# Optimization experiments

Measured on AMD Instinct MI355X. Metric: run time of the kernel, lower is better.

## Reference

```python
import jax, jax.numpy as jnp
import numpy as np

HIDDEN = 1000
IN_DIM = 1024


def setup_inputs() -> dict:
    key = jax.random.key(0)
    ks = jax.random.split(key, 9)
    s = 0.05
    return {
        "x": jax.random.normal(ks[0], (64, 128, IN_DIM), dtype=jnp.float32),
        "W1": jax.random.normal(ks[1], (IN_DIM, 4 * HIDDEN), dtype=jnp.float32) * s,
        "U1": jax.random.normal(ks[2], (HIDDEN, 4 * HIDDEN), dtype=jnp.float32) * s,
        "b1": jnp.zeros((4 * HIDDEN,), dtype=jnp.float32),
        "W2": jax.random.normal(ks[3], (HIDDEN, 4 * HIDDEN), dtype=jnp.float32) * s,
        "U2": jax.random.normal(ks[4], (HIDDEN, 4 * HIDDEN), dtype=jnp.float32) * s,
        "b2": jnp.zeros((4 * HIDDEN,), dtype=jnp.float32),
        "Wo": jax.random.normal(ks[5], (HIDDEN, 6), dtype=jnp.float32) * s,
        "bo": jnp.zeros((6,), dtype=jnp.float32),
    }


def _lstm_step(h, c, z):
    # Keras LSTMCell gate order: i, f, g(cell), o
    i, f, g, o = jnp.split(z, 4, axis=-1)
    i = jax.nn.sigmoid(i)
    f = jax.nn.sigmoid(f)
    o = jax.nn.sigmoid(o)
    c_new = f * c + i * jnp.tanh(g)
    h_new = o * jnp.tanh(c_new)
    return h_new, c_new


def reference(x, W1, U1, b1, W2, U2, b2, Wo, bo):
    B = x.shape[0]
    xs = jnp.swapaxes(x, 0, 1)  # [T, B, D]

    def step(carry, xt):
        h1, c1, h2, c2 = carry
        z1 = xt @ W1 + h1 @ U1 + b1
        h1, c1 = _lstm_step(h1, c1, z1)
        z2 = h1 @ W2 + h2 @ U2 + b2
        h2, c2 = _lstm_step(h2, c2, z2)
        return (h1, c1, h2, c2), None

    zeros = jnp.zeros((B, HIDDEN), dtype=x.dtype)
    (h1, c1, h2, c2), _ = jax.lax.scan(step, (zeros, zeros, zeros, zeros), xs)
    # RNN(return_sequences=False) returns last top-cell hidden state
    return h2 @ Wo + bo
```

## Files before the change

kernel.cpp:

```cpp
#include <hip/hip_runtime.h>
#include <hip/hip_bf16.h>

#define TT 128
#define DD 1024
#define HH 1000
#define NBLK 252
#define RING 16

typedef float f32x4 __attribute__((ext_vector_type(4)));
typedef __bf16 bf16x8 __attribute__((ext_vector_type(8)));

__device__ __forceinline__ bf16x8 asbf(f32x4 v) { return __builtin_bit_cast(bf16x8, v); }

__device__ __forceinline__ void ld_a(bf16x8* d, const char* p) {
    asm volatile("global_load_dwordx4 %0, %1, off sc0" : "=v"(*d) : "v"(p));
}
__device__ __forceinline__ void st_byp(char* p, bf16x8 v) {
    asm volatile("global_store_dwordx4 %0, %1, off sc0 sc1" :: "v"(p), "v"(v) : "memory");
}
__device__ __forceinline__ void st_ctl(unsigned* p, unsigned v) {
    asm volatile("global_store_dword %0, %1, off sc0 sc1" :: "v"(p), "v"(v) : "memory");
}

#define AT_RLX __ATOMIC_RELAXED
#define SC_AGT __HIP_MEMORY_SCOPE_AGENT

__global__ void zero_ws(unsigned int* __restrict__ p, int nwords) {
    int i = blockIdx.x * blockDim.x + threadIdx.x;
    if (i < nwords) p[i] = 0u;
}

__global__ void cast_x(const float* __restrict__ x, __bf16* __restrict__ xfh) {
    int gid = blockIdx.x * 256 + threadIdx.x;
    int lane = gid & 63;
    int mt = (gid >> 6) & 3;
    int ks = (gid >> 8) & 31;
    int t  = gid >> 13;
    int row = mt * 16 + (lane & 15);
    int k0  = ks * 32 + (lane >> 4) * 8;
    const float* sp = x + ((size_t)row * TT + t) * 1024 + k0;
    float4 v0 = *(const float4*)sp;
    float4 v1 = *(const float4*)(sp + 4);
    float f[8] = {v0.x, v0.y, v0.z, v0.w, v1.x, v1.y, v1.z, v1.w};
    bf16x8 hv;
#pragma unroll
    for (int j = 0; j < 8; ++j) hv[j] = (__bf16)f[j];
    ((bf16x8*)xfh)[gid] = hv;
}

__global__ __launch_bounds__(256) void pack_w2(
    const float* __restrict__ W1, const float* __restrict__ U1,
    const float* __restrict__ W2, const float* __restrict__ U2,
    __bf16* __restrict__ w1h, __bf16* __restrict__ w2h)
{
    int nt = blockIdx.x;
    int layer = blockIdx.y;
    const float* R1 = layer ? W2 : W1;
    const float* R2 = layer ? U2 : U1;
    int k1v = layer ? HH : 1024;
    __bf16* dh = layer ? w2h : w1h;
    int tid = threadIdx.x;

    __shared__ float lt[64][21];

    int kk = tid >> 2, g = tid & 3;
    for (int c = 0; c < 32; ++c) {
        int k = c * 64 + kk;
        float4 v = {0.f, 0.f, 0.f, 0.f};
        if (k < 1024) {
            if (k < k1v) v = *(const float4*)(R1 + (size_t)k * 4000 + g * 1000 + nt * 4);
        } else {
            int k2 = k - 1024;
            if (k2 < HH) v = *(const float4*)(R2 + (size_t)k2 * 4000 + g * 1000 + nt * 4);
        }
        lt[kk][g * 4 + 0] = v.x; lt[kk][g * 4 + 1] = v.y;
        lt[kk][g * 4 + 2] = v.z; lt[kk][g * 4 + 3] = v.w;
        __syncthreads();
        if (tid < 128) {
            int kbl = tid >> 4, col = tid & 15;
            int li = (col & 3) * 4 + (col >> 2);
            bf16x8 hv;
#pragma unroll
            for (int j = 0; j < 8; ++j) hv[j] = (__bf16)lt[kbl * 8 + j][li];
            size_t unit = ((size_t)nt * 256 + c * 8 + kbl) * 16 + col;
            ((bf16x8*)dh)[unit] = hv;
        }
        __syncthreads();
    }
}

__global__ __launch_bounds__(256, 1) void lstm_persist(
    const __bf16* __restrict__ xfh,
    const __bf16* __restrict__ w1h, const __bf16* __restrict__ w2h,
    const float* __restrict__ b1, const float* __restrict__ b2,
    __bf16* hbuf, unsigned int* ctrl)
{
    unsigned* xcdm    = ctrl + 32;
    unsigned* xcdFlag = ctrl + 384;
    unsigned* arr     = ctrl + 512;

    const int bid = blockIdx.x;
    const int layer = bid >= 126;
    const int r0 = layer ? bid - 126 : bid;
    const int bh = r0 >= 63;
    const int nb = bh ? r0 - 63 : r0;
    const int tid = threadIdx.x;
    const int lane = tid & 63, w = tid >> 6;
    const int op = w >> 1, kh = w & 1;
    const int ln = lane & 15, kg = lane >> 4;

    const char* h1ring = (const char*)hbuf;
    const char* h2ring = (const char*)(hbuf + (size_t)RING * 65536);

    __shared__ unsigned s_ldr;
    if (tid == 0) {
        unsigned x;
        asm volatile("s_getreg_b32 %0, hwreg(HW_REG_XCC_ID)" : "=s"(x));
        x &= 7u;
        unsigned old = __hip_atomic_fetch_add(&xcdm[x], 1u, AT_RLX, SC_AGT);
        s_ldr = (x << 8) | (old == 0u ? 1u : 0u);
    }

    const f32x4* wfh = (const f32x4*)(layer ? w2h : w1h);
    f32x4 WH[64];
#pragma unroll
    for (int tl = 0; tl < 4; ++tl) {
        int nt = nb * 4 + tl; if (nt > 249) nt = 249;
#pragma unroll
        for (int ks = 0; ks < 16; ++ks) {
            int kb = op * 128 + kh * 64 + ks * 4 + kg;
            WH[tl * 16 + ks] = wfh[((size_t)nt * 256 + kb) * 16 + ln];
        }
    }
#define PIN8(p0,p1,p2,p3,p4,p5,p6,p7) \
    asm volatile("" : "+a"(p0),"+a"(p1),"+a"(p2),"+a"(p3),"+a"(p4),"+a"(p5),"+a"(p6),"+a"(p7))
    PIN8(WH[0],WH[1],WH[2],WH[3],WH[4],WH[5],WH[6],WH[7]);
    PIN8(WH[8],WH[9],WH[10],WH[11],WH[12],WH[13],WH[14],WH[15]);
    PIN8(WH[16],WH[17],WH[18],WH[19],WH[20],WH[21],WH[22],WH[23]);
    PIN8(WH[24],WH[25],WH[26],WH[27],WH[28],WH[29],WH[30],WH[31]);
    PIN8(WH[32],WH[33],WH[34],WH[35],WH[36],WH[37],WH[38],WH[39]);
    PIN8(WH[40],WH[41],WH[42],WH[43],WH[44],WH[45],WH[46],WH[47]);
    PIN8(WH[48],WH[49],WH[50],WH[51],WH[52],WH[53],WH[54],WH[55]);
    PIN8(WH[56],WH[57],WH[58],WH[59],WH[60],WH[61],WH[62],WH[63]);
#undef PIN8

    const float* bias = layer ? b2 : b1;
    float bias_q[2][4];
#pragma unroll
    for (int q = 0; q < 2; ++q) {
        int task = tid * 2 + q;
        int n = nb * 16 + (task & 15); if (n > HH - 1) n = HH - 1;
#pragma unroll
        for (int g = 0; g < 4; ++g) bias_q[q][g] = bias[(size_t)g * HH + n];
    }
    float creg[2] = {0.f, 0.f};

    __shared__ float zs[2][32][68];
    __shared__ float hs[32][17];
    __syncthreads();

#pragma unroll 1
    for (int t = 0; t <= TT; ++t) {
        const bool active = layer ? (t >= 1) : (t <= TT - 1);
        if (active) {
            const char *pAh;
            char *poh;
            if (layer == 0) {
                if (op == 0) pAh = (const char*)xfh + (size_t)t * 131072;
                else         pAh = h1ring + (size_t)((t - 1) & (RING - 1)) * 131072;
                poh = (char*)(h1ring + (size_t)(t & (RING - 1)) * 131072);
            } else {
                if (op == 0) pAh = h1ring + (size_t)((t - 1) & (RING - 1)) * 131072;
                else         pAh = h2ring + (size_t)((t - 2) & (RING - 1)) * 131072;
                poh = (char*)(h2ring + (size_t)((t - 1) & (RING - 1)) * 131072);
            }
            pAh += ((size_t)kh * 4096 + bh * 128 + lane) * 16;

            f32x4 acc[4][2];
#pragma unroll
            for (int tl = 0; tl < 4; ++tl)
#pragma unroll
                for (int mt = 0; mt < 2; ++mt) acc[tl][mt] = (f32x4){0.f, 0.f, 0.f, 0.f};

            bf16x8 rh[8][2];
#define LDB(s, k) do { _Pragma("unroll") \
    for (int mt = 0; mt < 2; ++mt) \
        ld_a(&rh[s][mt], pAh + (size_t)((k) * 256 + mt * 64) * 16); \
    } while (0)
#define CPK(k, s) do { _Pragma("unroll") \
    for (int tl = 0; tl < 4; ++tl) { \
        bf16x8 wh_ = asbf(WH[tl * 16 + (k)]); \
        _Pragma("unroll") \
        for (int mt = 0; mt < 2; ++mt) \
            acc[tl][mt] = __builtin_amdgcn_mfma_f32_16x16x32_bf16(rh[s][mt], wh_, acc[tl][mt], 0, 0, 0); \
    } } while (0)

            LDB(0, 0); LDB(1, 1); LDB(2, 2); LDB(3, 3);
            LDB(4, 4); LDB(5, 5); LDB(6, 6); LDB(7, 7);
#pragma unroll
            for (int ks = 0; ks < 16; ++ks) {
                if (ks <= 8)       asm volatile("s_waitcnt vmcnt(14)" ::: "memory");
                else if (ks == 9)  asm volatile("s_waitcnt vmcnt(12)" ::: "memory");
                else if (ks == 10) asm volatile("s_waitcnt vmcnt(10)" ::: "memory");
                else if (ks == 11) asm volatile("s_waitcnt vmcnt(8)"  ::: "memory");
                else if (ks == 12) asm volatile("s_waitcnt vmcnt(6)"  ::: "memory");
                else if (ks == 13) asm volatile("s_waitcnt vmcnt(4)"  ::: "memory");
                else if (ks == 14) asm volatile("s_waitcnt vmcnt(2)"  ::: "memory");
                else               asm volatile("s_waitcnt vmcnt(0)"  ::: "memory");
                __builtin_amdgcn_sched_barrier(0);
                CPK(ks, ks & 7);
                if (ks < 8) LDB(ks & 7, ks + 8);
            }
#undef LDB
#undef CPK

            if (kh == 0) {
#pragma unroll
                for (int tl = 0; tl < 4; ++tl)
#pragma unroll
                    for (int mt = 0; mt < 2; ++mt)
#pragma unroll
                        for (int r = 0; r < 4; ++r)
                            zs[op][mt * 16 + kg * 4 + r][tl * 16 + ln] = acc[tl][mt][r];
            }
            __syncthreads();
            if (kh == 1) {
#pragma unroll
                for (int tl = 0; tl < 4; ++tl)
#pragma unroll
                    for (int mt = 0; mt < 2; ++mt)
#pragma unroll
                        for (int r = 0; r < 4; ++r)
                            zs[op][mt * 16 + kg * 4 + r][tl * 16 + ln] += acc[tl][mt][r];
            }
            __syncthreads();

#pragma unroll
            for (int q = 0; q < 2; ++q) {
                int task = tid * 2 + q;
                int b = task >> 4, cl = task & 15;
                int cc = (cl >> 2) * 16 + (cl & 3) * 4;
                float zg[4];
#pragma unroll
                for (int g = 0; g < 4; ++g)
                    zg[g] = zs[0][b][cc + g] + zs[1][b][cc + g] + bias_q[q][g];
                float ig = 1.f / (1.f + __expf(-zg[0]));
                float fg = 1.f / (1.f + __expf(-zg[1]));
                float gg = 1.f - 2.f / (__expf(2.f * zg[2]) + 1.f);
                float og = 1.f / (1.f + __expf(-zg[3]));
                float cn = fg * creg[q] + ig * gg;
                creg[q] = cn;
                hs[b][cl] = og * (1.f - 2.f / (__expf(2.f * cn) + 1.f));
            }
            __syncthreads();

            if (tid < 64) {
                int lnn = tid & 15;
                int mt_l = (tid >> 4) & 1;
                int kgsel = tid >> 5;
                if (nb * 16 + kgsel * 8 < HH) {
                    bf16x8 hv;
#pragma unroll
                    for (int j = 0; j < 8; ++j)
                        hv[j] = (__bf16)hs[mt_l * 16 + lnn][kgsel * 8 + j];
                    size_t unit = (((size_t)(nb >> 1) * 4 + bh * 2 + mt_l) * 64)
                                + ((nb & 1) * 2 + kgsel) * 16 + lnn;
                    st_byp(poh + unit * 16, hv);
                }
            }
        }

        if (t < TT) {
            const unsigned tp1 = (unsigned)(t + 1);
            if (w == 0) {
                asm volatile("s_waitcnt vmcnt(0)" ::: "memory");
                if (tid == 0) st_ctl(arr + (size_t)bid * 4, tp1);
                const unsigned* a0 = arr + (size_t)lane * 4;
                bool done = false;
                while (!done) {
                    unsigned v0, v1, v2, v3;
                    asm volatile("global_load_dword %0, %1, off sc0 sc1" : "=v"(v0) : "v"(a0));
                    asm volatile("global_load_dword %0, %1, off sc0 sc1" : "=v"(v1) : "v"(a0 + 256));
                    asm volatile("global_load_dword %0, %1, off sc0 sc1" : "=v"(v2) : "v"(a0 + 512));
                    asm volatile("global_load_dword %0, %1, off sc0 sc1" : "=v"(v3) : "v"(a0 + 768));
                    asm volatile("s_waitcnt vmcnt(0)" ::: "memory");
                    bool ok = (v0 >= tp1) && (v1 >= tp1) && (v2 >= tp1)
                           && ((lane + 192 >= NBLK) || (v3 >= tp1));
                    done = __all(ok);
                    if (!done) __builtin_amdgcn_s_sleep(1);
                }
                if ((tp1 & (RING - 1u)) == 0u) {
                    if (tid == 0) {
                        unsigned info = s_ldr;
                        unsigned* fP = xcdFlag + (info >> 8) * 16;
                        if (info & 1u) {
                            __builtin_amdgcn_fence(__ATOMIC_ACQUIRE, "agent");
                            asm volatile("s_waitcnt vmcnt(0) lgkmcnt(0)" ::: "memory");
                            __hip_atomic_store(fP, tp1, AT_RLX, SC_AGT);
                        } else {
                            while (__hip_atomic_load(fP, AT_RLX, SC_AGT) < tp1)
                                __builtin_amdgcn_s_sleep(1);
                        }
                    }
                    __builtin_amdgcn_wave_barrier();
                }
            }
            __syncthreads();
        }
    }
}

__global__ void out_proj(const __bf16* __restrict__ h2h,
                         const float* __restrict__ Wo, const float* __restrict__ bo,
                         float* __restrict__ out)
{
    int b = blockIdx.x, tid = threadIdx.x;
    int mt = b >> 4, ln = b & 15;
    float acc[6] = {0, 0, 0, 0, 0, 0};
    for (int n = tid; n < HH; n += 256) {
        int ks = n >> 5, kg = (n >> 3) & 3, j = n & 7;
        size_t idx = (((size_t)ks * 4 + mt) * 64 + kg * 16 + ln) * 8 + j;
        float h = (float)h2h[idx];
#pragma unroll
        for (int o = 0; o < 6; ++o) acc[o] += h * Wo[n * 6 + o];
    }
#pragma unroll
    for (int o = 0; o < 6; ++o)
        for (int off = 32; off; off >>= 1) acc[o] += __shfl_down(acc[o], off, 64);
    __shared__ float red[4][6];
    int lane = tid & 63, wv = tid >> 6;
    if (lane == 0) {
#pragma unroll
        for (int o = 0; o < 6; ++o) red[wv][o] = acc[o];
    }
    __syncthreads();
    if (tid < 6) {
        float s = bo[tid];
#pragma unroll
        for (int w = 0; w < 4; ++w) s += red[w][tid];
        out[b * 6 + tid] = s;
    }
}

extern "C" void kernel_launch(void* const* d_in, const int* in_sizes, int n_in,
                              void* d_out, int out_size, void* d_ws, size_t ws_size,
                              hipStream_t stream) {
    const float* x  = (const float*)d_in[0];
    const float* W1 = (const float*)d_in[1];
    const float* U1 = (const float*)d_in[2];
    const float* b1 = (const float*)d_in[3];
    const float* W2 = (const float*)d_in[4];
    const float* U2 = (const float*)d_in[5];
    const float* b2 = (const float*)d_in[6];
    const float* Wo = (const float*)d_in[7];
    const float* bo = (const float*)d_in[8];
    float* out = (float*)d_out;

    char* p = (char*)d_ws;
    __bf16* hbuf = (__bf16*)p; p += (size_t)2 * RING * 65536 * 2;
    unsigned int* ctrl = (unsigned int*)p; p += 8192;
    __bf16* xfh = (__bf16*)p; p += (size_t)8388608 * 2;
    __bf16* w1h = (__bf16*)p; p += (size_t)8192000 * 2;
    __bf16* w2h = (__bf16*)p; p += (size_t)8192000 * 2;

    zero_ws<<<4104, 256, 0, stream>>>((unsigned int*)d_ws, 1050624);
    cast_x<<<4096, 256, 0, stream>>>(x, xfh);
    pack_w2<<<dim3(250, 2), 256, 0, stream>>>(W1, U1, W2, U2, w1h, w2h);

    lstm_persist<<<NBLK, 256, 0, stream>>>(xfh, w1h, w2h, b1, b2, hbuf, ctrl);

    out_proj<<<64, 256, 0, stream>>>(hbuf + (size_t)(RING + 15) * 65536, Wo, bo, out);
}
```

Before: 739.6 us.

## Relax per-step global barrier to wait only on dependent block groups

Replaces the full grid barrier each timestep with a dependency-aware wait: a block waits for the current step only from the block groups whose hidden-state outputs it consumes, and accepts other blocks lagging by up to 14 steps. A full barrier is still enforced every RING-th step before the cross-XCD flag handshake. This cuts time spent waiting on unrelated blocks and lets layers pipeline, at the risk of ring-buffer overwrite hazards if the lag bound is wrong.

New measurement: 756.8 us. 1.02x slower.

```diff
diff --git a/kernel.cpp b/kernel.cpp
--- a/kernel.cpp
+++ b/kernel.cpp
@@ -159,6 +159,17 @@
     __shared__ float hs[32][17];
     __syncthreads();
 
+    const int gA0 = bh * 63, gA1 = gA0 + 63;
+    const int gB0 = layer ? 126 + bh * 63 : gA0;
+    const int gB1 = gB0 + 63;
+    bool dep_j[4], val_j[4];
+#pragma unroll
+    for (int j = 0; j < 4; ++j) {
+        int s = lane + 64 * j;
+        val_j[j] = s < NBLK;
+        dep_j[j] = (s >= gA0 && s < gA1) || (s >= gB0 && s < gB1);
+    }
+
 #pragma unroll 1
     for (int t = 0; t <= TT; ++t) {
         const bool active = layer ? (t >= 1) : (t <= TT - 1);
@@ -275,6 +286,7 @@
             if (w == 0) {
                 asm volatile("s_waitcnt vmcnt(0)" ::: "memory");
                 if (tid == 0) st_ctl(arr + (size_t)bid * 4, tp1);
+                const unsigned thr = tp1 > 14u ? tp1 - 14u : 0u;
                 const unsigned* a0 = arr + (size_t)lane * 4;
                 bool done = false;
                 while (!done) {
@@ -284,12 +296,27 @@
                     asm volatile("global_load_dword %0, %1, off sc0 sc1" : "=v"(v2) : "v"(a0 + 512));
                     asm volatile("global_load_dword %0, %1, off sc0 sc1" : "=v"(v3) : "v"(a0 + 768));
                     asm volatile("s_waitcnt vmcnt(0)" ::: "memory");
-                    bool ok = (v0 >= tp1) && (v1 >= tp1) && (v2 >= tp1)
-                           && ((lane + 192 >= NBLK) || (v3 >= tp1));
+                    bool ok = (!val_j[0] || (v0 >= thr && (!dep_j[0] || v0 >= tp1)))
+                           && (!val_j[1] || (v1 >= thr && (!dep_j[1] || v1 >= tp1)))
+                           && (!val_j[2] || (v2 >= thr && (!dep_j[2] || v2 >= tp1)))
+                           && (!val_j[3] || (v3 >= thr && (!dep_j[3] || v3 >= tp1)));
                     done = __all(ok);
                     if (!done) __builtin_amdgcn_s_sleep(1);
                 }
                 if ((tp1 & (RING - 1u)) == 0u) {
+                    bool gdone = false;
+                    while (!gdone) {
+                        unsigned v0, v1, v2, v3;
+                        asm volatile("global_load_dword %0, %1, off sc0 sc1" : "=v"(v0) : "v"(a0));
+                        asm volatile("global_load_dword %0, %1, off sc0 sc1" : "=v"(v1) : "v"(a0 + 256));
+                        asm volatile("global_load_dword %0, %1, off sc0 sc1" : "=v"(v2) : "v"(a0 + 512));
+                        asm volatile("global_load_dword %0, %1, off sc0 sc1" : "=v"(v3) : "v"(a0 + 768));
+                        asm volatile("s_waitcnt vmcnt(0)" ::: "memory");
+                        bool ok = (!val_j[0] || v0 >= tp1) && (!val_j[1] || v1 >= tp1)
+                               && (!val_j[2] || v2 >= tp1) && (!val_j[3] || v3 >= tp1);
+                        gdone = __all(ok);
+                        if (!gdone) __builtin_amdgcn_s_sleep(1);
+                    }
                     if (tid == 0) {
                         unsigned info = s_ldr;
                         unsigned* fP = xcdFlag + (info >> 8) * 16;
```
